# Kernel tuning notes

Hardware: AMD Instinct MI355X
Metric: run time of the kernel (lower is better)

The kernel has to match this reference:

```python
import jax, jax.numpy as jnp
from jax import lax
import numpy as np

B, C, PC, OC = 2, 256, 256, 256
H = W = 128
F = 2            # downsample_fac -> qkv conv kernel/stride and head upsample factor
NH, D = 4, C // 4  # 4 heads, attn_size = in_c//4
EPS = 1e-5


def conv2d(x, w, b, stride, padding):
    y = lax.conv_general_dilated(x, w, (stride, stride), padding,
                                 dimension_numbers=('NCHW', 'OIHW', 'NCHW'))
    return y + b[None, :, None, None]


def upsample_nearest(x, f):
    return jnp.repeat(jnp.repeat(x, f, axis=2), f, axis=3)


def setup_inputs() -> dict:
    key = jax.random.key(0)
    ks = jax.random.split(key, 16)
    s = 0.02  # small weight scale for numeric stability
    return {
        'app_enc':      jax.random.normal(ks[0], (B, C, H, W), jnp.float32),
        'app_pose_enc': jax.random.normal(ks[1], (B, C, H, W), jnp.float32),
        'pose_enc':     jax.random.normal(ks[2], (B, C, H, W), jnp.float32),
        'prev_inp':     jax.random.normal(ks[3], (B, PC, H // 2, W // 2), jnp.float32),
        'qw': jax.random.normal(ks[4], (NH, D, C, F, F), jnp.float32) * s,
        'qb': jax.random.normal(ks[5], (NH, D), jnp.float32) * s,
        'kw': jax.random.normal(ks[6], (NH, D, C, F, F), jnp.float32) * s,
        'kb': jax.random.normal(ks[7], (NH, D), jnp.float32) * s,
        'vw': jax.random.normal(ks[8], (NH, D, C, F, F), jnp.float32) * s,
        'vb': jax.random.normal(ks[9], (NH, D), jnp.float32) * s,
        'gamma': jax.random.normal(ks[10], (NH,), jnp.float32) * 0.1,
        'fw': jax.random.normal(ks[11], (C, 2 * C, 1, 1), jnp.float32) * s,
        'fb': jax.random.normal(ks[12], (C,), jnp.float32) * s,
        'cw': jax.random.normal(ks[13], (OC, C + PC, 3, 3), jnp.float32) * s,
        'cb': jax.random.normal(ks[14], (OC,), jnp.float32) * s,
    }


def reference(app_enc, app_pose_enc, pose_enc, prev_inp,
              qw, qb, kw, kb, vw, vb, gamma, fw, fb, cw, cb):
    # ---- AttnMech: 4 heads, q/k/v via stride-F convs over stacked heads ----
    def heads_proj(x, w, b):
        y = conv2d(x, w.reshape(NH * D, C, F, F), b.reshape(NH * D), F, 'VALID')
        _, _, h2, w2 = y.shape
        return y.reshape(B, NH, D, h2 * w2), h2, w2

    q, h2, w2 = heads_proj(pose_enc, qw, qb)        # [B,NH,D,N]
    k, _, _ = heads_proj(app_pose_enc, kw, kb)
    v, _, _ = heads_proj(app_enc, vw, vb)

    # unnormalized (no softmax) scaled dot-product attention, N = h2*w2
    attn = jnp.einsum('bhdn,bhdm->bhnm', q, k) / jnp.sqrt(jnp.float32(D))
    out = jnp.einsum('bhnm,bhdm->bhdn', attn, v)    # [B,NH,D,N]
    out = out.reshape(B, NH, D, h2, w2) * gamma[None, :, None, None, None]
    out = upsample_nearest(out.reshape(B, NH * D, h2, w2), F)  # back to [B,C,H,W]

    cat = jnp.concatenate([pose_enc, out], axis=1)  # [B, 2C, H, W]
    x = conv2d(cat, fw, fb, 1, 'VALID')             # 1x1 final_conv -> [B,C,H,W]

    # ---- GenDecAttnBlock tail: upsample prev, concat, ConvBlock ----
    prev = upsample_nearest(prev_inp, 2)            # [B,PC,H,W]
    x = jnp.concatenate([x, prev], axis=1)          # [B, C+PC, H, W]
    y = conv2d(x, cw, cb, 1, 'SAME')                # 3x3, pad 1
    mean = y.mean(axis=(2, 3), keepdims=True)
    var = y.var(axis=(2, 3), keepdims=True)         # biased, as torch InstanceNorm2d
    y = (y - mean) / jnp.sqrt(var + EPS)
    return jax.nn.relu(y)
```

## Files before the change

### kernel.cpp

```cpp
#include <hip/hip_runtime.h>
#include <hip/hip_bf16.h>

#define N2   4096
#define HWP  16384
#define EPSI 1e-5f

typedef unsigned short ushort_t;
typedef __attribute__((ext_vector_type(8))) short short8;
typedef __attribute__((ext_vector_type(4))) float f32x4;

static const size_t BUF0_OFF  = 0;
static const size_t BUF1_OFF  = 4194304;
static const size_t QT_OFF    = 8388608;
static const size_t KC_OFF    = 9437184;
static const size_t VC_OFF    = 10485760;
static const size_t S_OFF     = 11534336;
static const size_t SUM_OFF   = 11567104;
static const size_t SUM2_OFF  = 11567616;
static const size_t ZP_OFF    = 11568128;
static const size_t XCAT_OFF  = 11568192;
static const size_t PREVT_OFF = 15762496;
static const size_t WQ_OFF    = 16811072;
static const size_t WK_OFF    = 16942144;
static const size_t WV_OFF    = 17073216;
static const size_t WF_OFF    = 17204288;
static const size_t WA3X_OFF  = 17269824;
static const size_t WPP_OFF   = 17564736;
static const size_t Y3_OFF    = BUF1_OFF;

__device__ __forceinline__ ushort_t f2bf(float x) {
    union { float f; unsigned u; } v; v.f = x;
    unsigned r = v.u + 0x7FFFu + ((v.u >> 16) & 1u);
    return (ushort_t)(r >> 16);
}
__device__ __forceinline__ float bf2f(ushort_t h) {
    union { unsigned u; float f; } v; v.u = ((unsigned)h) << 16; return v.f;
}
__device__ __forceinline__ void gload_lds16(const void* g, void* l) {
    __builtin_amdgcn_global_load_lds(
        (const __attribute__((address_space(1))) void*)g,
        (__attribute__((address_space(3))) void*)l, 16, 0, 0);
}

__global__ __launch_bounds__(256) void prep_k(const float* __restrict__ qw,
                                              const float* __restrict__ kw,
                                              const float* __restrict__ vw,
                                              const float* __restrict__ fw,
                                              const float* __restrict__ cw,
                                              const float* __restrict__ prev,
                                              float* __restrict__ wsf) {
    __shared__ ushort_t T[64][64];
    int sec = blockIdx.y, bx = blockIdx.x, t = threadIdx.x;
    if (sec < 3) {
        if (bx >= 256) return;
        int idx = bx * 256 + t;
        const float* src = sec == 0 ? qw : (sec == 1 ? kw : vw);
        ushort_t* dst = (ushort_t*)(wsf + (sec == 0 ? WQ_OFF : (sec == 1 ? WK_OFF : WV_OFF)));
        float4 v = *(const float4*)&src[(size_t)idx * 4];
        dst[0 * 65536 + idx] = f2bf(v.x);
        dst[1 * 65536 + idx] = f2bf(v.y);
        dst[2 * 65536 + idx] = f2bf(v.z);
        dst[3 * 65536 + idx] = f2bf(v.w);
    } else if (sec == 3) {
        int idx = bx * 256 + t;
        ((ushort_t*)(wsf + WF_OFF))[idx] = f2bf(fw[idx]);
    } else if (sec == 4) {
        int idx = bx * 256 + t;
        int oc = idx >> 9, c = idx & 511;
        const float* src = cw + (size_t)idx * 9;
        float w[9];
#pragma unroll
        for (int tp = 0; tp < 9; ++tp) w[tp] = src[tp];
        if (c < 256) {
            ushort_t* wA3x = (ushort_t*)(wsf + WA3X_OFF);
#pragma unroll
            for (int tp = 0; tp < 9; ++tp)
                wA3x[((size_t)tp * 256 + oc) * 256 + c] = f2bf(w[tp]);
        } else {
            int cc = c - 256;
            ushort_t* wPP = (ushort_t*)(wsf + WPP_OFF);
#pragma unroll
            for (int py = 0; py < 2; ++py) {
                float rs[2][3];
#pragma unroll
                for (int fx = 0; fx < 3; ++fx) {
                    if (py == 0) { rs[0][fx] = w[fx];           rs[1][fx] = w[3 + fx] + w[6 + fx]; }
                    else         { rs[0][fx] = w[fx] + w[3 + fx]; rs[1][fx] = w[6 + fx]; }
                }
#pragma unroll
                for (int pxp = 0; pxp < 2; ++pxp)
#pragma unroll
                    for (int j2 = 0; j2 < 2; ++j2) {
                        float v0 = pxp == 0 ? rs[j2][0] : rs[j2][0] + rs[j2][1];
                        float v1 = pxp == 0 ? rs[j2][1] + rs[j2][2] : rs[j2][2];
                        wPP[(((size_t)((py * 2 + pxp) * 4 + j2 * 2 + 0)) * 256 + oc) * 256 + cc] = f2bf(v0);
                        wPP[(((size_t)((py * 2 + pxp) * 4 + j2 * 2 + 1)) * 256 + oc) * 256 + cc] = f2bf(v1);
                    }
            }
        }
    } else if (sec == 5) {
        int y2 = bx & 63, ct = (bx >> 6) & 3, b = bx >> 8;
        ushort_t* pT = (ushort_t*)(wsf + PREVT_OFF);
#pragma unroll
        for (int i = 0; i < 4; ++i) {
            int s = t + i * 256;
            int cc = s >> 4, xq = s & 15;
            float4 v = *(const float4*)&prev[(((size_t)b * 256 + ct * 64 + cc) * 64 + y2) * 64 + xq * 4];
            ushort4 h; h.x = f2bf(v.x); h.y = f2bf(v.y); h.z = f2bf(v.z); h.w = f2bf(v.w);
            *(ushort4*)&T[cc][xq * 4] = h;
        }
        __syncthreads();
#pragma unroll
        for (int i = 0; i < 2; ++i) {
            int w = t * 2 + i;
            int px = w >> 3, cbk = w & 7;
            short8 o;
#pragma unroll
            for (int j = 0; j < 8; ++j) o[j] = (short)T[cbk * 8 + j][px];
            *(short8*)&pT[((size_t)b * N2 + (size_t)y2 * 64 + px) * 256 + ct * 64 + cbk * 8] = o;
        }
    } else {
        int idx = bx * 256 + t;
        if (idx < 33856) wsf[S_OFF + idx] = 0.f;
    }
}

__device__ __forceinline__ void xpm_body(const float* __restrict__ in, ushort_t* __restrict__ xpm,
                                         int y, int ct, int b, int t) {
    __shared__ ushort_t T[64][128];
#pragma unroll
    for (int i = 0; i < 8; ++i) {
        int s = t + i * 256;
        int cc = s >> 5, xq = s & 31;
        float4 v = *(const float4*)&in[(((size_t)b * 256 + ct * 64 + cc) * 128 + y) * 128 + xq * 4];
        ushort4 h; h.x = f2bf(v.x); h.y = f2bf(v.y); h.z = f2bf(v.z); h.w = f2bf(v.w);
        *(ushort4*)&T[cc][xq * 4] = h;
    }
    __syncthreads();
#pragma unroll
    for (int i = 0; i < 4; ++i) {
        int w = t * 4 + i;
        int px = w >> 3, cbk = w & 7;
        short8 o;
#pragma unroll
        for (int j = 0; j < 8; ++j) o[j] = (short)T[cbk * 8 + j][px];
        *(short8*)&xpm[(((size_t)b * HWP) + (size_t)y * 128 + px) * 256 + ct * 64 + cbk * 8] = o;
    }
}

__global__ __launch_bounds__(256) void xpm2_k(const float* __restrict__ app,
                                              const float* __restrict__ app_pose,
                                              float* __restrict__ wsf) {
    int z = blockIdx.z, which = z >> 1, b = z & 1;
    const float* in = which == 0 ? app : app_pose;
    ushort_t* dst = (ushort_t*)(wsf + (which == 0 ? BUF0_OFF : BUF1_OFF));
    xpm_body(in, dst, blockIdx.x, blockIdx.y, b, threadIdx.x);
}

__global__ __launch_bounds__(256) void xpmP_k(const float* __restrict__ pose,
                                              float* __restrict__ wsf) {
    xpm_body(pose, (ushort_t*)(wsf + BUF0_OFF), blockIdx.x, blockIdx.y, blockIdx.z, threadIdx.x);
}

template<int MODE>
__device__ __forceinline__ void qkv_body(int nb, int oct, int b,
                                         const float* __restrict__ bias,
                                         const float* __restrict__ gamma,
                                         const ushort_t* __restrict__ wA,
                                         const ushort_t* __restrict__ xpm,
                                         ushort_t* __restrict__ outp) {
    int n0 = nb * 32, oc0 = oct * 128;
    __shared__ alignas(16) ushort_t As[2][128 * 64];
    __shared__ alignas(16) ushort_t Bs[2][32 * 64];
    int t = threadIdx.x, lane = t & 63, wv = t >> 6;
    int wm = wv >> 1, wn = wv & 1, l15 = lane & 15, lq = lane >> 4;
    f32x4 acc[4] = {};

    auto stage = [&](int chunk, int bufi) {
        int tap = chunk >> 2, c0 = (chunk & 3) << 6;
        int fy = tap >> 1, fx = tap & 1;
#pragma unroll
        for (int r = 0; r < 4; ++r) {
            int slot = t + r * 256;
            int row = slot >> 3, cbk = slot & 7;
            const ushort_t* src = wA + ((size_t)tap * 65536 + (size_t)(oc0 + row) * 256
                                        + c0 + ((cbk ^ (row & 7)) << 3));
            gload_lds16(src, (ushort_t*)As[bufi] + (((size_t)wv * 64 + r * 256) << 3));
        }
        {
            int n = t >> 3, cbk = t & 7;
            int ng = n0 + n;
            int iy = ((ng >> 6) << 1) + fy, ix = ((ng & 63) << 1) + fx;
            const ushort_t* src = xpm + (((size_t)b * HWP + (size_t)iy * 128 + ix) * 256
                                         + c0 + ((cbk ^ (n & 7)) << 3));
            gload_lds16(src, (ushort_t*)Bs[bufi] + ((size_t)wv * 64 << 3));
        }
    };

    stage(0, 0);
    __syncthreads();
    int buf = 0;
    for (int chunk = 0; chunk < 16; ++chunk) {
        short8 af[4][2], bf[2];
#pragma unroll
        for (int m = 0; m < 4; ++m) {
            int row = wm * 64 + m * 16 + l15;
#pragma unroll
            for (int ks = 0; ks < 2; ++ks)
                af[m][ks] = *(const short8*)&As[buf][row * 64 + (((ks * 4 + lq) ^ (row & 7)) << 3)];
        }
        {
            int col = wn * 16 + l15;
#pragma unroll
            for (int ks = 0; ks < 2; ++ks)
                bf[ks] = *(const short8*)&Bs[buf][col * 64 + (((ks * 4 + lq) ^ (col & 7)) << 3)];
        }
        if (chunk < 15) stage(chunk + 1, buf ^ 1);
#pragma unroll
        for (int ks = 0; ks < 2; ++ks)
#pragma unroll
            for (int m = 0; m < 4; ++m)
                acc[m] = __builtin_amdgcn_mfma_f32_16x16x32_bf16(af[m][ks], bf[ks], acc[m], 0, 0, 0);
        __syncthreads();
        buf ^= 1;
    }
#pragma unroll
    for (int m = 0; m < 4; ++m) {
        int col = wn * 16 + l15;
        int ng = n0 + col;
        int ocq = oc0 + wm * 64 + m * 16 + lq * 4;
        if (MODE == 0) {
            ushort4 o;
            float s0 = gamma[ocq >> 6] * 0.125f;
            o.x = f2bf((acc[m][0] + bias[ocq + 0]) * s0);
            o.y = f2bf((acc[m][1] + bias[ocq + 1]) * s0);
            o.z = f2bf((acc[m][2] + bias[ocq + 2]) * s0);
            o.w = f2bf((acc[m][3] + bias[ocq + 3]) * s0);
            *(ushort4*)&outp[((size_t)b * N2 + ng) * 256 + ocq] = o;
        } else {
#pragma unroll
            for (int r = 0; r < 4; ++r)
                outp[((size_t)(b * 256 + ocq + r)) * N2 + ng] = f2bf(acc[m][r] + bias[ocq + r]);
        }
    }
}

__global__ __launch_bounds__(256, 4) void kv_mfma(const float* __restrict__ kb_,
                                                  const float* __restrict__ vb_,
                                                  float* __restrict__ wsf) {
    int z = blockIdx.z, cv = z >> 1, b = z & 1;
    const ushort_t* wA  = (const ushort_t*)(wsf + (cv == 0 ? WV_OFF : WK_OFF));
    const ushort_t* xpm = (const ushort_t*)(wsf + (cv == 0 ? BUF0_OFF : BUF1_OFF));
    const float* bias   = cv == 0 ? vb_ : kb_;
    ushort_t* outp      = (ushort_t*)(wsf + (cv == 0 ? VC_OFF : KC_OFF));
    qkv_body<1>(blockIdx.x, blockIdx.y, b, bias, nullptr, wA, xpm, outp);
}

__global__ __launch_bounds__(256, 4) void q_mfma(const float* __restrict__ qb_,
                                                 const float* __restrict__ gamma,
                                                 float* __restrict__ wsf) {
    qkv_body<0>(blockIdx.x, blockIdx.y, blockIdx.z, qb_, gamma,
                (const ushort_t*)(wsf + WQ_OFF), (const ushort_t*)(wsf + BUF0_OFF),
                (ushort_t*)(wsf + QT_OFF));
}

__global__ __launch_bounds__(64) void attn_S_mfma(float* __restrict__ wsf) {
    int mc = blockIdx.x, bh = blockIdx.y;
    int b = bh >> 2, h = bh & 3;
    const ushort_t* vp = (const ushort_t*)(wsf + VC_OFF) + (size_t)(b * 256 + h * 64) * N2;
    const ushort_t* kp = (const ushort_t*)(wsf + KC_OFF) + (size_t)(b * 256 + h * 64) * N2;
    float* Sp = wsf + S_OFF + (size_t)bh * 4096;
    int lane = threadIdx.x, l15 = lane & 15, lq = lane >> 4;
    f32x4 acc[4][4] = {};
    for (int m0 = mc * 128; m0 < mc * 128 + 128; m0 += 32) {
        short8 af[4], bf[4];
#pragma unroll
        for (int mt = 0; mt < 4; ++mt)
            af[mt] = *(const short8*)&vp[(size_t)(mt * 16 + l15) * N2 + m0 + lq * 8];
#pragma unroll
        for (int nt = 0; nt < 4; ++nt)
            bf[nt] = *(const short8*)&kp[(size_t)(nt * 16 + l15) * N2 + m0 + lq * 8];
#pragma unroll
        for (int mt = 0; mt < 4; ++mt)
#pragma unroll
            for (int nt = 0; nt < 4; ++nt)
                acc[mt][nt] = __builtin_amdgcn_mfma_f32_16x16x32_bf16(
                    af[mt], bf[nt], acc[mt][nt], 0, 0, 0);
    }
#pragma unroll
    for (int mt = 0; mt < 4; ++mt)
#pragma unroll
        for (int nt = 0; nt < 4; ++nt)
#pragma unroll
            for (int r = 0; r < 4; ++r)
                atomicAdd(&Sp[(mt * 16 + lq * 4 + r) * 64 + nt * 16 + l15], acc[mt][nt][r]);
}

__global__ __launch_bounds__(256) void attn_O_mfma(float* __restrict__ wsf) {
    int nb = blockIdx.x, bh = blockIdx.y;
    int b = bh >> 2, h = bh & 3;
    const float* Sp = wsf + S_OFF + (size_t)bh * 4096;
    const ushort_t* qT = (const ushort_t*)(wsf + QT_OFF);
    ushort_t* attT = (ushort_t*)(wsf + KC_OFF);
    __shared__ ushort_t Sl[64][72];
    int t = threadIdx.x;
#pragma unroll
    for (int g = 0; g < 4; ++g) {
        int idx = t * 16 + g * 4;
        float4 v = *(const float4*)&Sp[idx];
        int row = idx >> 6, col = idx & 63;
        ushort4 o; o.x = f2bf(v.x); o.y = f2bf(v.y); o.z = f2bf(v.z); o.w = f2bf(v.w);
        *(ushort4*)&Sl[row][col] = o;
    }
    __syncthreads();
    int lane = t & 63, wv = t >> 6, l15 = lane & 15, lq = lane >> 4;
    int n_base = nb * 256 + wv * 64;
    f32x4 acc[4][4] = {};
#pragma unroll
    for (int ks = 0; ks < 2; ++ks) {
        short8 aS[4], bq[4];
#pragma unroll
        for (int mt = 0; mt < 4; ++mt)
            aS[mt] = *(const short8*)&Sl[mt * 16 + l15][ks * 32 + lq * 8];
#pragma unroll
        for (int nt = 0; nt < 4; ++nt)
            bq[nt] = *(const short8*)&qT[((size_t)b * N2 + n_base + nt * 16 + l15) * 256
                                         + h * 64 + ks * 32 + lq * 8];
#pragma unroll
        for (int mt = 0; mt < 4; ++mt)
#pragma unroll
            for (int nt = 0; nt < 4; ++nt)
                acc[mt][nt] = __builtin_amdgcn_mfma_f32_16x16x32_bf16(
                    aS[mt], bq[nt], acc[mt][nt], 0, 0, 0);
    }
#pragma unroll
    for (int mt = 0; mt < 4; ++mt)
#pragma unroll
        for (int nt = 0; nt < 4; ++nt) {
            int n = n_base + nt * 16 + l15;
            ushort4 o;
            o.x = f2bf(acc[mt][nt][0]); o.y = f2bf(acc[mt][nt][1]);
            o.z = f2bf(acc[mt][nt][2]); o.w = f2bf(acc[mt][nt][3]);
            *(ushort4*)&attT[((size_t)b * N2 + n) * 256 + h * 64 + mt * 16 + lq * 4] = o;
        }
}

__global__ __launch_bounds__(256, 3) void conv1x1_mfma(const float* __restrict__ fb,
                                                       float* __restrict__ wsf) {
    int lin = blockIdx.x;
    int swz = (lin & 7) * 128 + (lin >> 3);
    int xh = swz & 1, y = (swz >> 1) & 127, oct = (swz >> 8) & 1, b = swz >> 9;
    int oc0 = oct * 128, x0 = xh * 64;
    const ushort_t* wF   = (const ushort_t*)(wsf + WF_OFF);
    const ushort_t* xpm  = (const ushort_t*)(wsf + BUF0_OFF);
    const ushort_t* attT = (const ushort_t*)(wsf + KC_OFF);
    ushort_t* xcatT      = (ushort_t*)(wsf + XCAT_OFF);

    __shared__ alignas(16) ushort_t As[2][128 * 64];
    __shared__ alignas(16) ushort_t Bs[2][64 * 64];
    int t = threadIdx.x, lane = t & 63, wv = t >> 6;
    int wm = wv >> 1, wn = wv & 1, l15 = lane & 15, lq = lane >> 4;
    f32x4 acc[4][2] = {};

    auto stage = [&](int chunk, int bufi) {
        int c0 = chunk << 6;
#pragma unroll
        for (int r = 0; r < 4; ++r) {
            int slot = t + r * 256;
            int row = slot >> 3, cbk = slot & 7;
            const ushort_t* src = wF + ((size_t)(oc0 + row) * 512 + c0 + ((cbk ^ (row & 7)) << 3));
            gload_lds16(src, (ushort_t*)As[bufi] + (((size_t)wv * 64 + r * 256) << 3));
        }
#pragma unroll
        for (int r = 0; r < 2; ++r) {
            int slot = t + r * 256;
            int n = slot >> 3, cbk = slot & 7;
            int x = x0 + n;
            int sw = (cbk ^ (n & 7)) << 3;
            const ushort_t* src;
            if (c0 < 256)
                src = xpm + (((size_t)b * HWP + (size_t)y * 128 + x) * 256 + c0 + sw);
            else
                src = attT + (((size_t)b * N2 + (size_t)(y >> 1) * 64 + (x >> 1)) * 256
                              + (c0 - 256) + sw);
            gload_lds16(src, (ushort_t*)Bs[bufi] + (((size_t)wv * 64 + r * 256) << 3));
        }
    };

    stage(0, 0);
    __syncthreads();
    int buf = 0;
    for (int chunk = 0; chunk < 8; ++chunk) {
        short8 af[4][2], bf[2][2];
#pragma unroll
        for (int m = 0; m < 4; ++m) {
            int row = wm * 64 + m * 16 + l15;
#pragma unroll
            for (int ks = 0; ks < 2; ++ks)
                af[m][ks] = *(const short8*)&As[buf][row * 64 + (((ks * 4 + lq) ^ (row & 7)) << 3)];
        }
#pragma unroll
        for (int n = 0; n < 2; ++n) {
            int col = wn * 32 + n * 16 + l15;
#pragma unroll
            for (int ks = 0; ks < 2; ++ks)
                bf[n][ks] = *(const short8*)&Bs[buf][col * 64 + (((ks * 4 + lq) ^ (col & 7)) << 3)];
        }
        if (chunk < 7) stage(chunk + 1, buf ^ 1);
#pragma unroll
        for (int ks = 0; ks < 2; ++ks)
#pragma unroll
            for (int m = 0; m < 4; ++m)
#pragma unroll
                for (int n = 0; n < 2; ++n)
                    acc[m][n] = __builtin_amdgcn_mfma_f32_16x16x32_bf16(
                        af[m][ks], bf[n][ks], acc[m][n], 0, 0, 0);
        __syncthreads();
        buf ^= 1;
    }
#pragma unroll
    for (int m = 0; m < 4; ++m)
#pragma unroll
        for (int n = 0; n < 2; ++n) {
            int col = x0 + wn * 32 + n * 16 + l15;
            int ocq = oc0 + wm * 64 + m * 16 + lq * 4;
            ushort4 o;
            o.x = f2bf(acc[m][n][0] + fb[ocq + 0]);
            o.y = f2bf(acc[m][n][1] + fb[ocq + 1]);
            o.z = f2bf(acc[m][n][2] + fb[ocq + 2]);
            o.w = f2bf(acc[m][n][3] + fb[ocq + 3]);
            *(ushort4*)&xcatT[((size_t)b * HWP + (size_t)y * 128 + col) * 256 + ocq] = o;
        }
}

__global__ __launch_bounds__(256, 2) void conv3x3_mfma(const float* __restrict__ cb,
                                                       float* __restrict__ wsf) {
    int lin = blockIdx.x;
    int swz = (lin & 7) * 64 + (lin >> 3);
    int y = swz & 127, oct = (swz >> 7) & 1, b = swz >> 8;
    int oc0 = oct * 128;
    int py = y & 1, yh = y >> 1;

    const ushort_t* xcatT = (const ushort_t*)(wsf + XCAT_OFF);
    const ushort_t* prevT = (const ushort_t*)(wsf + PREVT_OFF);
    const ushort_t* wA3x  = (const ushort_t*)(wsf + WA3X_OFF);
    const ushort_t* wPP   = (const ushort_t*)(wsf + WPP_OFF);
    const ushort_t* zp    = (const ushort_t*)(wsf + ZP_OFF);
    ushort_t* y3          = (ushort_t*)(wsf + Y3_OFF);

    __shared__ alignas(16) ushort_t As[2 * 128 * 64];
    __shared__ alignas(16) ushort_t Bs[128 * 64];
    int t = threadIdx.x, lane = t & 63, wv = t >> 6;
    int wm = wv >> 1, wn = wv & 1, l15 = lane & 15, lq = lane >> 4;
    f32x4 acc[4][4] = {};

    for (int chunk = 0; chunk < 52; ++chunk) {
        bool isPrev = chunk >= 36;
        if (!isPrev) {
            int tap = chunk >> 2, c0 = (chunk & 3) << 6;
            int fy = tap / 3, fx = tap - fy * 3;
            int yy = y + fy - 1;
#pragma unroll
            for (int r = 0; r < 4; ++r) {
                int slot = t + r * 256;
                int row = slot >> 3, cbk = slot & 7;
                const ushort_t* src = wA3x + (((size_t)tap * 256 + oc0 + row) * 256
                                              + c0 + ((cbk ^ (row & 7)) << 3));
                gload_lds16(src, (ushort_t*)As + (((size_t)wv * 64 + r * 256) << 3));
            }
#pragma unroll
            for (int r = 0; r < 4; ++r) {
                int slot = t + r * 256;
                int n = slot >> 3, cbk = slot & 7;
                int x = 2 * (n & 63) + (n >> 6);
                int xx = x + fx - 1;
                int sw = (cbk ^ (n & 7)) << 3;
                bool ok = (yy >= 0) && (yy < 128) && (xx >= 0) && (xx < 128);
                const ushort_t* src = ok
                    ? xcatT + (((size_t)b * HWP + (size_t)yy * 128 + xx) * 256 + c0 + sw)
                    : zp;
                gload_lds16(src, (ushort_t*)Bs + (((size_t)wv * 64 + r * 256) << 3));
            }
        } else {
            int pi = chunk - 36;
            int tap4 = pi >> 2, c0 = (pi & 3) << 6;
            int j2 = tap4 >> 1, i2 = tap4 & 1;
            int pr = yh + py + j2 - 1;
#pragma unroll
            for (int r = 0; r < 8; ++r) {
                int slot = t + r * 256;
                int p = slot >> 10, rem = slot & 1023;
                int row = rem >> 3, cbk = rem & 7;
                const ushort_t* src = wPP + (((size_t)((py * 2 + p) * 4 + tap4) * 256
                                              + oc0 + row) * 256 + c0 + ((cbk ^ (row & 7)) << 3));
                gload_lds16(src, (ushort_t*)As + (((size_t)wv * 64 + r * 256) << 3));
            }
#pragma unroll
            for (int r = 0; r < 4; ++r) {
                int slot = t + r * 256;
                int n = slot >> 3, cbk = slot & 7;
                int pc = (n & 63) - 1 + i2 + (n >> 6);
                int sw = (cbk ^ (n & 7)) << 3;
                bool ok = (pr >= 0) && (pr < 64) && (pc >= 0) && (pc < 64);
                const ushort_t* src = ok
                    ? prevT + (((size_t)b * N2 + (size_t)pr * 64 + pc) * 256 + c0 + sw)
                    : zp;
                gload_lds16(src, (ushort_t*)Bs + (((size_t)wv * 64 + r * 256) << 3));
            }
        }
        __syncthreads();
        int abase = isPrev ? wn * 8192 : 0;
#pragma unroll
        for (int ks = 0; ks < 2; ++ks) {
            short8 af[4], bf[4];
#pragma unroll
            for (int m = 0; m < 4; ++m) {
                int row = wm * 64 + m * 16 + l15;
                af[m] = *(const short8*)&As[abase + row * 64 + (((ks * 4 + lq) ^ (row & 7)) << 3)];
            }
#pragma unroll
            for (int n = 0; n < 4; ++n) {
                int col = wn * 64 + n * 16 + l15;
                bf[n] = *(const short8*)&Bs[col * 64 + (((ks * 4 + lq) ^ (col & 7)) << 3)];
            }
#pragma unroll
            for (int m = 0; m < 4; ++m)
#pragma unroll
                for (int n = 0; n < 4; ++n)
                    acc[m][n] = __builtin_amdgcn_mfma_f32_16x16x32_bf16(
                        af[m], bf[n], acc[m][n], 0, 0, 0);
        }
        __syncthreads();
    }

#pragma unroll
    for (int m = 0; m < 4; ++m)
#pragma unroll
        for (int n = 0; n < 4; ++n) {
            int col = wn * 64 + n * 16 + l15;
            int x = 2 * (col & 63) + (col >> 6);
            size_t pxo = (size_t)y * 128 + x;
#pragma unroll
            for (int r = 0; r < 4; ++r) {
                int oc = oc0 + wm * 64 + m * 16 + lq * 4 + r;
                y3[((size_t)b * 256 + oc) * HWP + pxo] = f2bf(acc[m][n][r] + cb[oc]);
            }
        }
}

__global__ __launch_bounds__(256) void inorm_relu_k(const float* __restrict__ wsf,
                                                    float* __restrict__ out) {
    int bc = blockIdx.x;
    const ushort_t* yp = (const ushort_t*)(wsf + Y3_OFF) + (size_t)bc * HWP;
    int t = threadIdx.x;
    float s1 = 0.f, s2 = 0.f;
#pragma unroll
    for (int i = 0; i < 8; ++i) {
        short8 v = *(const short8*)&yp[(size_t)(t + i * 256) * 8];
#pragma unroll
        for (int j = 0; j < 8; ++j) {
            float f = bf2f((ushort_t)v[j]);
            s1 += f; s2 += f * f;
        }
    }
#pragma unroll
    for (int o = 32; o; o >>= 1) {
        s1 += __shfl_xor(s1, o, 64);
        s2 += __shfl_xor(s2, o, 64);
    }
    __shared__ float r1[4], r2[4];
    if ((t & 63) == 0) { r1[t >> 6] = s1; r2[t >> 6] = s2; }
    __syncthreads();
    float S1 = r1[0] + r1[1] + r1[2] + r1[3];
    float S2 = r2[0] + r2[1] + r2[2] + r2[3];
    float mean = S1 * (1.f / HWP);
    float var  = S2 * (1.f / HWP) - mean * mean;
    float inv  = rsqrtf(var + EPSI);
    float* op = out + (size_t)bc * HWP;
#pragma unroll
    for (int i = 0; i < 8; ++i) {
        int base = (t + i * 256) * 8;
        short8 v = *(const short8*)&yp[(size_t)base];
        float4 o0, o1;
        o0.x = fmaxf((bf2f((ushort_t)v[0]) - mean) * inv, 0.f);
        o0.y = fmaxf((bf2f((ushort_t)v[1]) - mean) * inv, 0.f);
        o0.z = fmaxf((bf2f((ushort_t)v[2]) - mean) * inv, 0.f);
        o0.w = fmaxf((bf2f((ushort_t)v[3]) - mean) * inv, 0.f);
        o1.x = fmaxf((bf2f((ushort_t)v[4]) - mean) * inv, 0.f);
        o1.y = fmaxf((bf2f((ushort_t)v[5]) - mean) * inv, 0.f);
        o1.z = fmaxf((bf2f((ushort_t)v[6]) - mean) * inv, 0.f);
        o1.w = fmaxf((bf2f((ushort_t)v[7]) - mean) * inv, 0.f);
        *(float4*)&op[base]     = o0;
        *(float4*)&op[base + 4] = o1;
    }
}

extern "C" void kernel_launch(void* const* d_in, const int* in_sizes, int n_in,
                              void* d_out, int out_size, void* d_ws, size_t ws_size,
                              hipStream_t stream)
{
    (void)in_sizes; (void)n_in; (void)out_size; (void)ws_size;
    const float* app_enc  = (const float*)d_in[0];
    const float* app_pose = (const float*)d_in[1];
    const float* pose_enc = (const float*)d_in[2];
    const float* prev_inp = (const float*)d_in[3];
    const float* qw = (const float*)d_in[4];
    const float* qb = (const float*)d_in[5];
    const float* kw = (const float*)d_in[6];
    const float* kb = (const float*)d_in[7];
    const float* vw = (const float*)d_in[8];
    const float* vb = (const float*)d_in[9];
    const float* gamma = (const float*)d_in[10];
    const float* fw = (const float*)d_in[11];
    const float* fb = (const float*)d_in[12];
    const float* cw = (const float*)d_in[13];
    const float* cb = (const float*)d_in[14];
    float* ws  = (float*)d_ws;
    float* out = (float*)d_out;

    prep_k<<<dim3(512, 7), 256, 0, stream>>>(qw, kw, vw, fw, cw, prev_inp, ws);
    xpm2_k<<<dim3(128, 4, 4), 256, 0, stream>>>(app_enc, app_pose, ws);
    kv_mfma<<<dim3(128, 2, 4), 256, 0, stream>>>(kb, vb, ws);
    attn_S_mfma<<<dim3(32, 8), 64, 0, stream>>>(ws);
    xpmP_k<<<dim3(128, 4, 2), 256, 0, stream>>>(pose_enc, ws);
    q_mfma<<<dim3(128, 2, 2), 256, 0, stream>>>(qb, gamma, ws);
    attn_O_mfma<<<dim3(16, 8), 256, 0, stream>>>(ws);
    conv1x1_mfma<<<1024, 256, 0, stream>>>(fb, ws);
    conv3x3_mfma<<<512, 256, 0, stream>>>(cb, ws);
    inorm_relu_k<<<512, 256, 0, stream>>>(ws, out);
}
```

Measured before the change: 180.6 us.

## Fold attention matrix into final conv weights and fuse norm stats

Reassociates the attention output path. Instead of materialising att = S·q per pixel, a small kernel multiplies the attention half of the 1x1 final-conv weights by S^T to form a per-batch weight matrix M. The 1x1 conv then reads q directly against M, so the per-pixel attention output is never written or read back. Separately, the 3x3 conv epilogue accumulates per-channel sum and sum-of-squares with shuffles and atomics, so the instance-norm kernel skips its statistics pass over y3. This relies on the SUM buffers being zeroed beforehand. Stats are now taken from pre-rounding fp32 values and summed by atomics in nondeterministic order.

```diff
diff --git a/kernel.cpp b/kernel.cpp
--- a/kernel.cpp
+++ b/kernel.cpp
@@ -27,6 +27,7 @@
 static const size_t WA3X_OFF  = 17269824;
 static const size_t WPP_OFF   = 17564736;
 static const size_t Y3_OFF    = BUF1_OFF;
+static const size_t M_OFF     = KC_OFF;
 
 __device__ __forceinline__ ushort_t f2bf(float x) {
     union { float f; unsigned u; } v; v.f = x;
@@ -296,52 +297,55 @@
                 atomicAdd(&Sp[(mt * 16 + lq * 4 + r) * 64 + nt * 16 + l15], acc[mt][nt][r]);
 }
 
-__global__ __launch_bounds__(256) void attn_O_mfma(float* __restrict__ wsf) {
-    int nb = blockIdx.x, bh = blockIdx.y;
+__global__ __launch_bounds__(256) void attn_M_mfma(float* __restrict__ wsf) {
+    int bh = blockIdx.x;
     int b = bh >> 2, h = bh & 3;
     const float* Sp = wsf + S_OFF + (size_t)bh * 4096;
-    const ushort_t* qT = (const ushort_t*)(wsf + QT_OFF);
-    ushort_t* attT = (ushort_t*)(wsf + KC_OFF);
-    __shared__ ushort_t Sl[64][72];
+    const ushort_t* wF = (const ushort_t*)(wsf + WF_OFF);
+    ushort_t* M = (ushort_t*)(wsf + M_OFF);
+    __shared__ ushort_t SlT[64][72];
     int t = threadIdx.x;
 #pragma unroll
     for (int g = 0; g < 4; ++g) {
         int idx = t * 16 + g * 4;
         float4 v = *(const float4*)&Sp[idx];
-        int row = idx >> 6, col = idx & 63;
-        ushort4 o; o.x = f2bf(v.x); o.y = f2bf(v.y); o.z = f2bf(v.z); o.w = f2bf(v.w);
-        *(ushort4*)&Sl[row][col] = o;
+        int d = idx >> 6, dd = idx & 63;
+        SlT[dd + 0][d] = f2bf(v.x);
+        SlT[dd + 1][d] = f2bf(v.y);
+        SlT[dd + 2][d] = f2bf(v.z);
+        SlT[dd + 3][d] = f2bf(v.w);
     }
     __syncthreads();
     int lane = t & 63, wv = t >> 6, l15 = lane & 15, lq = lane >> 4;
-    int n_base = nb * 256 + wv * 64;
     f32x4 acc[4][4] = {};
 #pragma unroll
     for (int ks = 0; ks < 2; ++ks) {
-        short8 aS[4], bq[4];
-#pragma unroll
-        for (int mt = 0; mt < 4; ++mt)
-            aS[mt] = *(const short8*)&Sl[mt * 16 + l15][ks * 32 + lq * 8];
+        short8 aw[4], bs[4];
+#pragma unroll
+        for (int mt = 0; mt < 4; ++mt) {
+            int oc = wv * 64 + mt * 16 + l15;
+            aw[mt] = *(const short8*)&wF[(size_t)oc * 512 + 256 + h * 64 + ks * 32 + lq * 8];
+        }
 #pragma unroll
         for (int nt = 0; nt < 4; ++nt)
-            bq[nt] = *(const short8*)&qT[((size_t)b * N2 + n_base + nt * 16 + l15) * 256
-                                         + h * 64 + ks * 32 + lq * 8];
+            bs[nt] = *(const short8*)&SlT[nt * 16 + l15][ks * 32 + lq * 8];
 #pragma unroll
         for (int mt = 0; mt < 4; ++mt)
 #pragma unroll
             for (int nt = 0; nt < 4; ++nt)
                 acc[mt][nt] = __builtin_amdgcn_mfma_f32_16x16x32_bf16(
-                    aS[mt], bq[nt], acc[mt][nt], 0, 0, 0);
+                    aw[mt], bs[nt], acc[mt][nt], 0, 0, 0);
     }
 #pragma unroll
     for (int mt = 0; mt < 4; ++mt)
 #pragma unroll
         for (int nt = 0; nt < 4; ++nt) {
-            int n = n_base + nt * 16 + l15;
-            ushort4 o;
-            o.x = f2bf(acc[mt][nt][0]); o.y = f2bf(acc[mt][nt][1]);
-            o.z = f2bf(acc[mt][nt][2]); o.w = f2bf(acc[mt][nt][3]);
-            *(ushort4*)&attT[((size_t)b * N2 + n) * 256 + h * 64 + mt * 16 + lq * 4] = o;
+            int dd = nt * 16 + l15;
+#pragma unroll
+            for (int r = 0; r < 4; ++r) {
+                int oc = wv * 64 + mt * 16 + lq * 4 + r;
+                M[((size_t)b * 256 + oc) * 256 + h * 64 + dd] = f2bf(acc[mt][nt][r]);
+            }
         }
 }
 
@@ -352,8 +356,9 @@
     int xh = swz & 1, y = (swz >> 1) & 127, oct = (swz >> 8) & 1, b = swz >> 9;
     int oc0 = oct * 128, x0 = xh * 64;
     const ushort_t* wF   = (const ushort_t*)(wsf + WF_OFF);
+    const ushort_t* Mb   = (const ushort_t*)(wsf + M_OFF) + (size_t)b * 65536;
     const ushort_t* xpm  = (const ushort_t*)(wsf + BUF0_OFF);
-    const ushort_t* attT = (const ushort_t*)(wsf + KC_OFF);
+    const ushort_t* qT   = (const ushort_t*)(wsf + QT_OFF);
     ushort_t* xcatT      = (ushort_t*)(wsf + XCAT_OFF);
 
     __shared__ alignas(16) ushort_t As[2][128 * 64];
@@ -368,7 +373,10 @@
         for (int r = 0; r < 4; ++r) {
             int slot = t + r * 256;
             int row = slot >> 3, cbk = slot & 7;
-            const ushort_t* src = wF + ((size_t)(oc0 + row) * 512 + c0 + ((cbk ^ (row & 7)) << 3));
+            int sw = (cbk ^ (row & 7)) << 3;
+            const ushort_t* src;
+            if (c0 < 256) src = wF + ((size_t)(oc0 + row) * 512 + c0 + sw);
+            else          src = Mb + ((size_t)(oc0 + row) * 256 + (c0 - 256) + sw);
             gload_lds16(src, (ushort_t*)As[bufi] + (((size_t)wv * 64 + r * 256) << 3));
         }
 #pragma unroll
@@ -381,8 +389,8 @@
             if (c0 < 256)
                 src = xpm + (((size_t)b * HWP + (size_t)y * 128 + x) * 256 + c0 + sw);
             else
-                src = attT + (((size_t)b * N2 + (size_t)(y >> 1) * 64 + (x >> 1)) * 256
-                              + (c0 - 256) + sw);
+                src = qT + (((size_t)b * N2 + (size_t)(y >> 1) * 64 + (x >> 1)) * 256
+                            + (c0 - 256) + sw);
             gload_lds16(src, (ushort_t*)Bs[bufi] + (((size_t)wv * 64 + r * 256) << 3));
         }
     };
@@ -533,17 +541,31 @@
         __syncthreads();
     }
 
+    float* SUM  = wsf + SUM_OFF;
+    float* SUM2 = wsf + SUM2_OFF;
 #pragma unroll
     for (int m = 0; m < 4; ++m)
 #pragma unroll
-        for (int n = 0; n < 4; ++n) {
-            int col = wn * 64 + n * 16 + l15;
-            int x = 2 * (col & 63) + (col >> 6);
-            size_t pxo = (size_t)y * 128 + x;
-#pragma unroll
-            for (int r = 0; r < 4; ++r) {
-                int oc = oc0 + wm * 64 + m * 16 + lq * 4 + r;
-                y3[((size_t)b * 256 + oc) * HWP + pxo] = f2bf(acc[m][n][r] + cb[oc]);
+        for (int r = 0; r < 4; ++r) {
+            int oc = oc0 + wm * 64 + m * 16 + lq * 4 + r;
+            float bv = cb[oc];
+            float s1 = 0.f, s2 = 0.f;
+#pragma unroll
+            for (int n = 0; n < 4; ++n) {
+                float v = acc[m][n][r] + bv;
+                s1 += v; s2 += v * v;
+                int col = wn * 64 + n * 16 + l15;
+                int x = 2 * (col & 63) + (col >> 6);
+                y3[((size_t)b * 256 + oc) * HWP + (size_t)y * 128 + x] = f2bf(v);
+            }
+#pragma unroll
+            for (int o2 = 1; o2 < 16; o2 <<= 1) {
+                s1 += __shfl_xor(s1, o2, 64);
+                s2 += __shfl_xor(s2, o2, 64);
+            }
+            if (l15 == 0) {
+                atomicAdd(&SUM[b * 256 + oc], s1);
+                atomicAdd(&SUM2[b * 256 + oc], s2);
             }
         }
 }
@@ -552,31 +574,11 @@
                                                     float* __restrict__ out) {
     int bc = blockIdx.x;
     const ushort_t* yp = (const ushort_t*)(wsf + Y3_OFF) + (size_t)bc * HWP;
-    int t = threadIdx.x;
-    float s1 = 0.f, s2 = 0.f;
-#pragma unroll
-    for (int i = 0; i < 8; ++i) {
-        short8 v = *(const short8*)&yp[(size_t)(t + i * 256) * 8];
-#pragma unroll
-        for (int j = 0; j < 8; ++j) {
-            float f = bf2f((ushort_t)v[j]);
-            s1 += f; s2 += f * f;
-        }
-    }
-#pragma unroll
-    for (int o = 32; o; o >>= 1) {
-        s1 += __shfl_xor(s1, o, 64);
-        s2 += __shfl_xor(s2, o, 64);
-    }
-    __shared__ float r1[4], r2[4];
-    if ((t & 63) == 0) { r1[t >> 6] = s1; r2[t >> 6] = s2; }
-    __syncthreads();
-    float S1 = r1[0] + r1[1] + r1[2] + r1[3];
-    float S2 = r2[0] + r2[1] + r2[2] + r2[3];
-    float mean = S1 * (1.f / HWP);
-    float var  = S2 * (1.f / HWP) - mean * mean;
+    float mean = wsf[SUM_OFF + bc] * (1.f / HWP);
+    float var  = wsf[SUM2_OFF + bc] * (1.f / HWP) - mean * mean;
     float inv  = rsqrtf(var + EPSI);
     float* op = out + (size_t)bc * HWP;
+    int t = threadIdx.x;
 #pragma unroll
     for (int i = 0; i < 8; ++i) {
         int base = (t + i * 256) * 8;
@@ -624,7 +626,7 @@
     attn_S_mfma<<<dim3(32, 8), 64, 0, stream>>>(ws);
     xpmP_k<<<dim3(128, 4, 2), 256, 0, stream>>>(pose_enc, ws);
     q_mfma<<<dim3(128, 2, 2), 256, 0, stream>>>(qb, gamma, ws);
-    attn_O_mfma<<<dim3(16, 8), 256, 0, stream>>>(ws);
+    attn_M_mfma<<<8, 256, 0, stream>>>(ws);
     conv1x1_mfma<<<1024, 256, 0, stream>>>(fb, ws);
     conv3x3_mfma<<<512, 256, 0, stream>>>(cb, ws);
     inorm_relu_k<<<512, 256, 0, stream>>>(ws, out);
```

New measurement: 205.5 us. 13.8% more time.
